# Kernel tuning notes

Measured on AMD Instinct MI355X. Metric: run time of the kernel, lower is better.

Reference implementation:

```python
import jax, jax.numpy as jnp
import numpy as np

EPS = 1e-08
STRIDE = (1, 1, 1)
PAD = [(1, 1), (1, 1), (1, 1)]


def setup_inputs() -> dict:
    key = jax.random.key(0)
    k1, k2, k3, k4 = jax.random.split(key, 4)
    N, inC, outC, L = 4, 128, 128, 512
    D, H, W = 16, 64, 64
    x = jax.random.normal(k1, (N, inC, D, H, W), dtype=jnp.float32)
    latent = jax.random.normal(k2, (N, L), dtype=jnp.float32)
    weight = jax.random.normal(k3, (outC, inC, 3, 3, 3), dtype=jnp.float32) * 0.01
    fc_w = jax.random.normal(k4, (inC, L), dtype=jnp.float32) * (1.0 / np.sqrt(L))
    fc_b = jnp.zeros((inC,), dtype=jnp.float32)
    return {"x": x, "latent": latent, "weight": weight, "fc_w": fc_w, "fc_b": fc_b}


def _conv_one(xi, wi):
    # xi: [inC, D, H, W]; wi: [outC, inC, kD, kH, kW]
    out = jax.lax.conv_general_dilated(
        xi[None], wi, window_strides=STRIDE, padding=PAD,
        dimension_numbers=("NCDHW", "OIDHW", "NCDHW"))
    return out[0]  # [outC, D, H, W]


def reference(x, latent, weight, fc_w, fc_b):
    # style: [N, inC]
    style = latent @ fc_w.T + fc_b
    # per-sample modulated weights: [N, outC, inC, kD, kH, kW]
    w_mod = weight[None] * style[:, None, :, None, None, None]
    demod = jax.lax.rsqrt(jnp.sum(w_mod * w_mod, axis=(2, 3, 4, 5), keepdims=True) + EPS)
    w_mod = w_mod * demod
    # grouped conv with groups=N == per-sample conv, vectorized with vmap
    out = jax.vmap(_conv_one)(x, w_mod)  # [N, outC, D, H, W]
    return out
```

## Files before the change

kernel.cpp:

```cpp
#include <hip/hip_runtime.h>
#include <math.h>

#define NN 4
#define C 128
#define DD 16
#define HH 64
#define WW 64
#define LL 512
#define EPSF 1e-8f

typedef __attribute__((ext_vector_type(8)))  short short8;
typedef __attribute__((ext_vector_type(16))) float f32x16;

__device__ __forceinline__ unsigned short f2bf(float f) {
    unsigned u = __float_as_uint(f);
    unsigned r = (u + 0x7fffu + ((u >> 16) & 1u)) >> 16;
    return (unsigned short)r;
}
__device__ __forceinline__ float bf2f(unsigned short h) {
    return __uint_as_float(((unsigned)h) << 16);
}

__global__ __launch_bounds__(64) void k_style(const float* __restrict__ latent,
                                              const float* __restrict__ fc_w,
                                              const float* __restrict__ fc_b,
                                              float* __restrict__ style) {
    int b = blockIdx.x;
    int n = b >> 7, c = b & 127;
    int lane = threadIdx.x;
    const float* lat = latent + n * LL;
    const float* w   = fc_w   + c * LL;
    float s = 0.f;
    for (int l = lane; l < LL; l += 64) s += lat[l] * w[l];
    #pragma unroll
    for (int off = 32; off; off >>= 1) s += __shfl_down(s, off);
    if (lane == 0) style[b] = s + fc_b[c];
}

__global__ __launch_bounds__(128) void k_s2(const float* __restrict__ weight,
                                            float* __restrict__ s2) {
    int oc = blockIdx.x, ic = threadIdx.x;
    const float* src = weight + (oc * C + ic) * 27;
    float s = 0.f;
    #pragma unroll
    for (int t = 0; t < 27; ++t) { float v = src[t]; s += v * v; }
    s2[oc * C + ic] = s;
}

__global__ __launch_bounds__(64) void k_demod(const float* __restrict__ s2,
                                              const float* __restrict__ style,
                                              float* __restrict__ demod) {
    int b = blockIdx.x;
    int n = b >> 7, oc = b & 127;
    int lane = threadIdx.x;
    float s = 0.f;
    for (int ic = lane; ic < C; ic += 64) {
        float st = style[n * C + ic];
        s += s2[oc * C + ic] * st * st;
    }
    #pragma unroll
    for (int off = 32; off; off >>= 1) s += __shfl_down(s, off);
    if (lane == 0) demod[b] = rsqrtf(s + EPSF);
}

__global__ __launch_bounds__(256) void k_wt(const float* __restrict__ w,
                                            unsigned short* __restrict__ Wt) {
    int b = blockIdx.x;
    int kdh = b >> 3, cc = b & 7;
    int kd = kdh / 3, kh = kdh - 3 * kd;
    for (int e = threadIdx.x; e < 12288; e += 256) {
        int i  = e & 15;
        int oc = (e >> 4) & 127;
        int t  = e >> 11;
        int part = t / 3, kw = t - 3 * part;
        int ic = cc * 16 + i;
        float v = w[(oc * C + ic) * 27 + kd * 9 + kh * 3 + kw];
        unsigned short hv = f2bf(v);
        unsigned short ov = (part == 0) ? hv : f2bf(v - bf2f(hv));
        Wt[(size_t)b * 12288 + e] = ov;
    }
}

__global__ __launch_bounds__(256, 2) void k_conv(
        const float* __restrict__ x,
        const unsigned short* __restrict__ Wt,
        const float* __restrict__ style,
        const float* __restrict__ demod,
        float* __restrict__ out) {

    __shared__ __align__(16) unsigned short wld[2][3][C][16];
    __shared__ __align__(16) unsigned short xld[2][2][2][66][8];
    __shared__ float stl[C], dml[C];

    const int hb = blockIdx.x;
    const int d  = blockIdx.y;
    const int n  = blockIdx.z;
    const int h0 = hb * 2;
    const int tid  = threadIdx.x;
    const int lane = tid & 63;
    const int wv   = tid >> 6;
    const int wr   = wv >> 1;
    const int wc   = wv & 1;

    if (tid < C)            stl[tid]      = style[n * C + tid];
    else if (tid < 2 * C)   dml[tid - C]  = demod[n * C + tid - C];
    if (tid < 16) {
        int part = tid >> 3, row = (tid >> 2) & 1, icb = (tid >> 1) & 1, e = tid & 1;
        short8 z = (short8)0;
        *(short8*)&xld[part][row][icb][e ? 65 : 0][0] = z;
    }

    const int srow = tid >> 7;
    const int sicb = (tid >> 6) & 1;
    const int sw   = tid & 63;

    f32x16 acc[2][2] = {};

    const int l31  = lane & 31;
    const int kreg = lane >> 5;

    for (int kdh = 0; kdh < 9; ++kdh) {
        const int kd = kdh / 3, kh = kdh - 3 * kd;
        const int zd = d + kd - 1;
        const int zh = h0 + kh - 1 + srow;
        const bool valid = ((unsigned)zd < DD) && ((unsigned)zh < HH);
        const float* xrow = x + ((((size_t)n * C) * DD + zd) * HH + zh) * WW + sw;

        for (int cc = 0; cc < 8; ++cc) {
            __syncthreads();

            {
                const unsigned short* gW = Wt + (size_t)(kdh * 8 + cc) * 12288;
                unsigned short* wflat = &wld[0][0][0][0];
                #pragma unroll
                for (int c2 = 0; c2 < 6; ++c2) {
                    const int chunk = wv * 6 + c2;
                    const unsigned short* src = gW + chunk * 512 + lane * 8;
                    unsigned short* dst = wflat + chunk * 512;
                    __builtin_amdgcn_global_load_lds(
                        (const __attribute__((address_space(1))) unsigned int*)src,
                        (__attribute__((address_space(3))) unsigned int*)dst,
                        16, 0, 0);
                }
            }

            if (valid) {
                const float* xs = xrow + ((size_t)(cc * 16 + sicb * 8)) * (DD * HH * WW);
                const float* stp = &stl[cc * 16 + sicb * 8];
                short8 vh, vl;
                #pragma unroll
                for (int j = 0; j < 8; ++j) {
                    float v = xs[(size_t)j * (DD * HH * WW)] * stp[j];
                    unsigned short h = f2bf(v);
                    vh[j] = (short)h;
                    vl[j] = (short)f2bf(v - bf2f(h));
                }
                *(short8*)&xld[0][srow][sicb][1 + sw][0] = vh;
                *(short8*)&xld[1][srow][sicb][1 + sw][0] = vl;
            } else {
                short8 z = (short8)0;
                *(short8*)&xld[0][srow][sicb][1 + sw][0] = z;
                *(short8*)&xld[1][srow][sicb][1 + sw][0] = z;
            }
            __syncthreads();

            #pragma unroll
            for (int kw = 0; kw < 3; ++kw) {
                short8 a[2][2], b[2][2];
                #pragma unroll
                for (int o = 0; o < 2; ++o) {
                    const int oc = wr * 64 + o * 32 + l31;
                    a[o][0] = *(const short8*)&wld[0][kw][oc][kreg * 8];
                    a[o][1] = *(const short8*)&wld[1][kw][oc][kreg * 8];
                }
                #pragma unroll
                for (int p = 0; p < 2; ++p) {
                    const int wpos = p * 32 + l31 + kw;
                    b[p][0] = *(const short8*)&xld[0][wc][kreg][wpos][0];
                    b[p][1] = *(const short8*)&xld[1][wc][kreg][wpos][0];
                }
                #pragma unroll
                for (int o = 0; o < 2; ++o)
                    #pragma unroll
                    for (int p = 0; p < 2; ++p) {
                        acc[o][p] = __builtin_amdgcn_mfma_f32_32x32x16_bf16(
                                        a[o][0], b[p][0], acc[o][p], 0, 0, 0);
                        acc[o][p] = __builtin_amdgcn_mfma_f32_32x32x16_bf16(
                                        a[o][0], b[p][1], acc[o][p], 0, 0, 0);
                        acc[o][p] = __builtin_amdgcn_mfma_f32_32x32x16_bf16(
                                        a[o][1], b[p][0], acc[o][p], 0, 0, 0);
                    }
            }
        }
    }

    const int lhi = lane >> 5;
    const int h = h0 + wc;
    #pragma unroll
    for (int o = 0; o < 2; ++o) {
        #pragma unroll
        for (int r = 0; r < 16; ++r) {
            const int ocrow = (r & 3) + 8 * (r >> 2) + 4 * lhi;
            const int oc = wr * 64 + o * 32 + ocrow;
            const float dm = dml[oc];
            #pragma unroll
            for (int p = 0; p < 2; ++p) {
                const int wq = p * 32 + l31;
                out[((((size_t)n * C + oc) * DD + d) * HH + h) * WW + wq] =
                    acc[o][p][r] * dm;
            }
        }
    }
}

extern "C" void kernel_launch(void* const* d_in, const int* in_sizes, int n_in,
                              void* d_out, int out_size, void* d_ws, size_t ws_size,
                              hipStream_t stream) {
    const float* x      = (const float*)d_in[0];
    const float* latent = (const float*)d_in[1];
    const float* weight = (const float*)d_in[2];
    const float* fc_w   = (const float*)d_in[3];
    const float* fc_b   = (const float*)d_in[4];
    float* out = (float*)d_out;

    float* style = (float*)d_ws;
    float* demod = style + 512;
    float* s2    = demod + 512;
    unsigned short* Wt = (unsigned short*)(s2 + 16384);

    hipLaunchKernelGGL(k_style, dim3(NN * C), dim3(64), 0, stream,
                       latent, fc_w, fc_b, style);
    hipLaunchKernelGGL(k_s2,    dim3(C), dim3(C), 0, stream, weight, s2);
    hipLaunchKernelGGL(k_wt,    dim3(72), dim3(256), 0, stream, weight, Wt);
    hipLaunchKernelGGL(k_demod, dim3(NN * C), dim3(64), 0, stream,
                       s2, style, demod);
    hipLaunchKernelGGL(k_conv,  dim3(32, DD, NN), dim3(256), 0, stream,
                       x, Wt, style, demod, out);
}
```

Measured before the change: 771.8 us.

## Double-buffer x tile in LDS and load weights directly into registers

The conv main loop is flattened into 72 stages. The x tile is double-buffered in LDS, and the next stage's x values are prefetched into registers before the MFMAs of the current stage, then converted and stored after them. This leaves one barrier per stage instead of two. Weight fragments now come straight from global memory (L2-cached) into registers instead of being staged through LDS, which removes the LDS weight buffer but adds global-load latency and register pressure on the MFMA path.

```diff
diff --git a/kernel.cpp b/kernel.cpp
--- a/kernel.cpp
+++ b/kernel.cpp
@@ -8,16 +8,18 @@
 #define WW 64
 #define LL 512
 #define EPSF 1e-8f
-
+#define DHW (DD * HH * WW)
+
+typedef unsigned short ushort_t;
 typedef __attribute__((ext_vector_type(8)))  short short8;
 typedef __attribute__((ext_vector_type(16))) float f32x16;
 
-__device__ __forceinline__ unsigned short f2bf(float f) {
+__device__ __forceinline__ ushort_t f2bf(float f) {
     unsigned u = __float_as_uint(f);
     unsigned r = (u + 0x7fffu + ((u >> 16) & 1u)) >> 16;
-    return (unsigned short)r;
-}
-__device__ __forceinline__ float bf2f(unsigned short h) {
+    return (ushort_t)r;
+}
+__device__ __forceinline__ float bf2f(ushort_t h) {
     return __uint_as_float(((unsigned)h) << 16);
 }
 
@@ -64,7 +66,7 @@
 }
 
 __global__ __launch_bounds__(256) void k_wt(const float* __restrict__ w,
-                                            unsigned short* __restrict__ Wt) {
+                                            ushort_t* __restrict__ Wt) {
     int b = blockIdx.x;
     int kdh = b >> 3, cc = b & 7;
     int kd = kdh / 3, kh = kdh - 3 * kd;
@@ -75,22 +77,22 @@
         int part = t / 3, kw = t - 3 * part;
         int ic = cc * 16 + i;
         float v = w[(oc * C + ic) * 27 + kd * 9 + kh * 3 + kw];
-        unsigned short hv = f2bf(v);
-        unsigned short ov = (part == 0) ? hv : f2bf(v - bf2f(hv));
+        ushort_t hv = f2bf(v);
+        ushort_t ov = (part == 0) ? hv : f2bf(v - bf2f(hv));
         Wt[(size_t)b * 12288 + e] = ov;
     }
 }
 
 __global__ __launch_bounds__(256, 2) void k_conv(
         const float* __restrict__ x,
-        const unsigned short* __restrict__ Wt,
+        const ushort_t* __restrict__ Wt,
         const float* __restrict__ style,
         const float* __restrict__ demod,
         float* __restrict__ out) {
 
-    __shared__ __align__(16) unsigned short wld[2][3][C][16];
-    __shared__ __align__(16) unsigned short xld[2][2][2][66][8];
-    __shared__ float stl[C], dml[C];
+    __shared__ __align__(16) ushort_t xld[2][2][2][2][66][8];
+    __shared__ float stl[C];
+    __shared__ float dml[C];
 
     const int hb = blockIdx.x;
     const int d  = blockIdx.y;
@@ -101,106 +103,120 @@
     const int wv   = tid >> 6;
     const int wr   = wv >> 1;
     const int wc   = wv & 1;
-
-    if (tid < C)            stl[tid]      = style[n * C + tid];
-    else if (tid < 2 * C)   dml[tid - C]  = demod[n * C + tid - C];
-    if (tid < 16) {
-        int part = tid >> 3, row = (tid >> 2) & 1, icb = (tid >> 1) & 1, e = tid & 1;
-        short8 z = (short8)0;
-        *(short8*)&xld[part][row][icb][e ? 65 : 0][0] = z;
-    }
+    const int l31  = lane & 31;
+    const int kreg = lane >> 5;
 
     const int srow = tid >> 7;
     const int sicb = (tid >> 6) & 1;
     const int sw   = tid & 63;
 
+    if (tid < C)          stl[tid]     = style[n * C + tid];
+    else if (tid < 2 * C) dml[tid - C] = demod[n * C + tid - C];
+    if (tid < 32) {
+        int buf  = tid >> 4, part = (tid >> 3) & 1, row = (tid >> 2) & 1,
+            icb  = (tid >> 1) & 1, e = tid & 1;
+        *(short8*)&xld[buf][part][row][icb][e ? 65 : 0][0] = (short8)0;
+    }
+    __syncthreads();
+
     f32x16 acc[2][2] = {};
 
-    const int l31  = lane & 31;
-    const int kreg = lane >> 5;
-
-    for (int kdh = 0; kdh < 9; ++kdh) {
-        const int kd = kdh / 3, kh = kdh - 3 * kd;
-        const int zd = d + kd - 1;
-        const int zh = h0 + kh - 1 + srow;
+    {
+        const int zd = d - 1, zh = h0 - 1 + srow;
         const bool valid = ((unsigned)zd < DD) && ((unsigned)zh < HH);
-        const float* xrow = x + ((((size_t)n * C) * DD + zd) * HH + zh) * WW + sw;
-
-        for (int cc = 0; cc < 8; ++cc) {
-            __syncthreads();
-
-            {
-                const unsigned short* gW = Wt + (size_t)(kdh * 8 + cc) * 12288;
-                unsigned short* wflat = &wld[0][0][0][0];
-                #pragma unroll
-                for (int c2 = 0; c2 < 6; ++c2) {
-                    const int chunk = wv * 6 + c2;
-                    const unsigned short* src = gW + chunk * 512 + lane * 8;
-                    unsigned short* dst = wflat + chunk * 512;
-                    __builtin_amdgcn_global_load_lds(
-                        (const __attribute__((address_space(1))) unsigned int*)src,
-                        (__attribute__((address_space(3))) unsigned int*)dst,
-                        16, 0, 0);
-                }
-            }
-
-            if (valid) {
-                const float* xs = xrow + ((size_t)(cc * 16 + sicb * 8)) * (DD * HH * WW);
-                const float* stp = &stl[cc * 16 + sicb * 8];
-                short8 vh, vl;
-                #pragma unroll
-                for (int j = 0; j < 8; ++j) {
-                    float v = xs[(size_t)j * (DD * HH * WW)] * stp[j];
-                    unsigned short h = f2bf(v);
-                    vh[j] = (short)h;
-                    vl[j] = (short)f2bf(v - bf2f(h));
-                }
-                *(short8*)&xld[0][srow][sicb][1 + sw][0] = vh;
-                *(short8*)&xld[1][srow][sicb][1 + sw][0] = vl;
-            } else {
-                short8 z = (short8)0;
-                *(short8*)&xld[0][srow][sicb][1 + sw][0] = z;
-                *(short8*)&xld[1][srow][sicb][1 + sw][0] = z;
-            }
-            __syncthreads();
-
-            #pragma unroll
-            for (int kw = 0; kw < 3; ++kw) {
-                short8 a[2][2], b[2][2];
+        const float* base = x + ((((size_t)n * C + sicb * 8) * DD + zd) * HH + zh) * WW + sw;
+        float xr[8];
+        #pragma unroll
+        for (int j = 0; j < 8; ++j) xr[j] = valid ? base[(size_t)j * DHW] : 0.f;
+        float4 sa = *(float4*)&stl[sicb * 8];
+        float4 sb = *(float4*)&stl[sicb * 8 + 4];
+        float stv[8] = {sa.x, sa.y, sa.z, sa.w, sb.x, sb.y, sb.z, sb.w};
+        short8 vh, vl;
+        #pragma unroll
+        for (int j = 0; j < 8; ++j) {
+            float v = xr[j] * stv[j];
+            ushort_t hv = f2bf(v);
+            vh[j] = (short)hv;
+            vl[j] = (short)f2bf(v - bf2f(hv));
+        }
+        *(short8*)&xld[0][0][srow][sicb][1 + sw][0] = vh;
+        *(short8*)&xld[0][1][srow][sicb][1 + sw][0] = vl;
+    }
+    __syncthreads();
+
+    for (int s = 0; s < 72; ++s) {
+        const int cur = s & 1;
+        const int s1  = (s < 71) ? s + 1 : 71;
+
+        const int kdh1 = s1 >> 3, cc1 = s1 & 7;
+        const int kd1  = kdh1 / 3;
+        const int zd   = d + kd1 - 1;
+        const int zh   = h0 + (kdh1 - 3 * kd1) - 1 + srow;
+        const bool valid = ((unsigned)zd < DD) && ((unsigned)zh < HH);
+        const float* base = x + ((((size_t)n * C + cc1 * 16 + sicb * 8) * DD + zd) * HH + zh) * WW + sw;
+        float xr[8];
+        #pragma unroll
+        for (int j = 0; j < 8; ++j) xr[j] = valid ? base[(size_t)j * DHW] : 0.f;
+
+        {
+            const ushort_t* gWs = Wt + (size_t)s * 12288;
+            short8 ah[3][2], al[3][2];
+            #pragma unroll
+            for (int kw = 0; kw < 3; ++kw)
                 #pragma unroll
                 for (int o = 0; o < 2; ++o) {
-                    const int oc = wr * 64 + o * 32 + l31;
-                    a[o][0] = *(const short8*)&wld[0][kw][oc][kreg * 8];
-                    a[o][1] = *(const short8*)&wld[1][kw][oc][kreg * 8];
+                    const ushort_t* ab = gWs + (kw * C + wr * 64 + o * 32 + l31) * 16 + kreg * 8;
+                    ah[kw][o] = *(const short8*)ab;
+                    al[kw][o] = *(const short8*)(ab + 3 * C * 16);
                 }
+            #pragma unroll
+            for (int kw = 0; kw < 3; ++kw) {
+                short8 b0[2], b1[2];
                 #pragma unroll
                 for (int p = 0; p < 2; ++p) {
                     const int wpos = p * 32 + l31 + kw;
-                    b[p][0] = *(const short8*)&xld[0][wc][kreg][wpos][0];
-                    b[p][1] = *(const short8*)&xld[1][wc][kreg][wpos][0];
+                    b0[p] = *(const short8*)&xld[cur][0][wc][kreg][wpos][0];
+                    b1[p] = *(const short8*)&xld[cur][1][wc][kreg][wpos][0];
                 }
                 #pragma unroll
                 for (int o = 0; o < 2; ++o)
                     #pragma unroll
                     for (int p = 0; p < 2; ++p) {
                         acc[o][p] = __builtin_amdgcn_mfma_f32_32x32x16_bf16(
-                                        a[o][0], b[p][0], acc[o][p], 0, 0, 0);
+                                        ah[kw][o], b0[p], acc[o][p], 0, 0, 0);
                         acc[o][p] = __builtin_amdgcn_mfma_f32_32x32x16_bf16(
-                                        a[o][0], b[p][1], acc[o][p], 0, 0, 0);
+                                        ah[kw][o], b1[p], acc[o][p], 0, 0, 0);
                         acc[o][p] = __builtin_amdgcn_mfma_f32_32x32x16_bf16(
-                                        a[o][1], b[p][0], acc[o][p], 0, 0, 0);
+                                        al[kw][o], b0[p], acc[o][p], 0, 0, 0);
                     }
             }
         }
-    }
-
-    const int lhi = lane >> 5;
+
+        {
+            float4 sa = *(float4*)&stl[cc1 * 16 + sicb * 8];
+            float4 sb = *(float4*)&stl[cc1 * 16 + sicb * 8 + 4];
+            float stv[8] = {sa.x, sa.y, sa.z, sa.w, sb.x, sb.y, sb.z, sb.w};
+            short8 vh, vl;
+            #pragma unroll
+            for (int j = 0; j < 8; ++j) {
+                float v = xr[j] * stv[j];
+                ushort_t hv = f2bf(v);
+                vh[j] = (short)hv;
+                vl[j] = (short)f2bf(v - bf2f(hv));
+            }
+            *(short8*)&xld[cur ^ 1][0][srow][sicb][1 + sw][0] = vh;
+            *(short8*)&xld[cur ^ 1][1][srow][sicb][1 + sw][0] = vl;
+        }
+
+        __syncthreads();
+    }
+
     const int h = h0 + wc;
     #pragma unroll
     for (int o = 0; o < 2; ++o) {
         #pragma unroll
         for (int r = 0; r < 16; ++r) {
-            const int ocrow = (r & 3) + 8 * (r >> 2) + 4 * lhi;
+            const int ocrow = (r & 3) + 8 * (r >> 2) + 4 * kreg;
             const int oc = wr * 64 + o * 32 + ocrow;
             const float dm = dml[oc];
             #pragma unroll
@@ -226,7 +242,7 @@
     float* style = (float*)d_ws;
     float* demod = style + 512;
     float* s2    = demod + 512;
-    unsigned short* Wt = (unsigned short*)(s2 + 16384);
+    ushort_t* Wt = (ushort_t*)(s2 + 16384);
 
     hipLaunchKernelGGL(k_style, dim3(NN * C), dim3(64), 0, stream,
                        latent, fc_w, fc_b, style);
```

Result: slower. 846.6 us (+9.7%).
